# Kernel tuning notes

Hardware: AMD Instinct MI355X
Metric: run time of the kernel (lower is better)

The kernel has to match this reference:

```python
import jax, jax.numpy as jnp
import numpy as np

P_F, P_E = 64, 64
S_F, S_E = 64, 64
W_F, W_E = 32, 32
FH, FO = 256, 128
PR_F, PR_E = 32, 32
VI_F, VI_E = 32, 32
RE_F, RE_E = 32, 32
H1, H2 = 64, 32
GH, NHEADS = 32, 4
DH = PR_E + VI_E + RE_E + P_E + S_E  # 224, hypernetwork input dim
FUSE_IN = 2 * P_E + 2 * S_E + W_E    # 288
N_COLL = 200000
M_NODES = 2048


def setup_inputs() -> dict:
    key = jax.random.key(0)
    ks = jax.random.split(key, 40)
    rn = lambda k, s, sc=1.0: jax.random.normal(k, s, jnp.float32) * sc
    W = 0.05
    inp = {
        'x_u_profile': rn(ks[0], (1, P_F)),
        'x_u_shopping': rn(ks[1], (1, S_F)),
        'x_u_workplace': rn(ks[2], (1, W_F)),
        'x_u_colleague_p': rn(ks[3], (N_COLL, P_F)),
        'x_u_colleague_s': rn(ks[4], (N_COLL, S_F)),
        'x_h_property': rn(ks[5], (1, PR_F)),
        'x_h_vicinity': rn(ks[6], (1, VI_F)),
        'x_h_reachability': rn(ks[7], (1, RE_F)),
        'x_h_neighborhood_p': rn(ks[8], (M_NODES, P_F)),
        'x_h_neighborhood_s': rn(ks[9], (M_NODES, S_F)),
        'x_h_neighborhood_g': jax.random.randint(ks[10], (M_NODES, M_NODES), 0, 2, jnp.int32),
        'W_up': rn(ks[11], (P_F, P_E), W), 'b_up': jnp.zeros((P_E,), jnp.float32),
        'W_us': rn(ks[12], (S_F, S_E), W), 'b_us': jnp.zeros((S_E,), jnp.float32),
        'W_uw': rn(ks[13], (W_F, W_E), W), 'b_uw': jnp.zeros((W_E,), jnp.float32),
        'v_w': rn(ks[14], (2 * (P_E + S_E), 1), W),
        'W_f1': rn(ks[15], (FUSE_IN, FH), W), 'b_f1': jnp.zeros((FH,), jnp.float32),
        'W_f2': rn(ks[16], (FH, FO), W), 'b_f2': jnp.zeros((FO,), jnp.float32),
        'W_m1': rn(ks[17], (FO, DH * H1), W), 'b_m1': jnp.zeros((DH * H1,), jnp.float32),
        'W_m2': rn(ks[18], (FO, H1 * H2), W), 'b_m2': jnp.zeros((H1 * H2,), jnp.float32),
        'W_m3': rn(ks[19], (FO, H2), W), 'b_m3': jnp.zeros((H2,), jnp.float32),
        'W_hp': rn(ks[20], (PR_F, PR_E), W), 'b_hp': jnp.zeros((PR_E,), jnp.float32),
        'W_hv': rn(ks[21], (VI_F, VI_E), W), 'b_hv': jnp.zeros((VI_E,), jnp.float32),
        'W_hr': rn(ks[22], (RE_F, RE_E), W), 'b_hr': jnp.zeros((RE_E,), jnp.float32),
        'Wg': rn(ks[23], (NHEADS, P_E + S_E, GH), W),
        'ag': rn(ks[24], (NHEADS, 2 * GH, 1), W),
        'Wo': rn(ks[25], (NHEADS * GH, P_E + S_E), W),
        'ao': rn(ks[26], (2 * (P_E + S_E), 1), W),
    }
    return inp


def _forward(x_u_profile, x_u_shopping, x_u_workplace, x_u_colleague_p, x_u_colleague_s,
             x_h_property, x_h_vicinity, x_h_reachability,
             x_h_neighborhood_p, x_h_neighborhood_s,
             W_up, b_up, W_us, b_us, W_uw, b_uw, v_w,
             W_f1, b_f1, W_f2, b_f2,
             W_m1, b_m1, W_m2, b_m2, W_m3, b_m3,
             W_hp, b_hp, W_hv, b_hv, W_hr, b_hr,
             Wg, ag, Wo, ao, adj):
    celu, relu = jax.nn.celu, jax.nn.relu
    # user embeddings (batch = 1)
    u_p = celu(x_u_profile @ W_up + b_up)    # [1, P_E]
    u_s = celu(x_u_shopping @ W_us + b_us)   # [1, S_E]
    u_w = celu(x_u_workplace @ W_uw + b_uw)  # [1, W_E]
    # colleague embeddings (shared embedding weights)
    c_p = celu(x_u_colleague_p @ W_up + b_up)  # [N, P_E]
    c_s = celu(x_u_colleague_s @ W_us + b_us)  # [N, S_E]
    n = c_p.shape[0]
    # expand user (shopping, profile) to colleague set and attend
    exp = jnp.concatenate([jnp.broadcast_to(u_s, (n, S_E)),
                           jnp.broadcast_to(u_p, (n, P_E))], axis=1)
    concat = jnp.concatenate([exp, c_p, c_s], axis=1)        # [N, 2*(P_E+S_E)]
    atten = jax.nn.softmax(concat @ v_w, axis=0)             # [N, 1]
    coll = jnp.concatenate([c_p, c_s], axis=1)               # [N, P_E+S_E]
    x_coll = (atten.T @ coll) / n                            # [1, P_E+S_E]
    # user fusion
    fu = jnp.concatenate([u_p, u_s, u_w, x_coll], axis=1)    # [1, FUSE_IN]
    x_u = celu(celu(fu @ W_f1 + b_f1) @ W_f2 + b_f2)         # [1, FO]
    # hypernetwork-generated weights
    w1 = celu(x_u @ W_m1 + b_m1).reshape(DH, H1)
    w2 = celu(x_u @ W_m2 + b_m2).reshape(H1, H2)
    w3 = celu(x_u @ W_m3 + b_m3).reshape(H2, 1)
    # house embeddings
    h_p = celu(x_h_property @ W_hp + b_hp)
    h_v = celu(x_h_vicinity @ W_hv + b_hv)
    h_r = celu(x_h_reachability @ W_hr + b_hr)
    # neighborhood GAT over dense adjacency
    n_p = celu(x_h_neighborhood_p @ W_up + b_up)
    n_s = celu(x_h_neighborhood_s @ W_us + b_us)
    gx = jnp.concatenate([n_p, n_s], axis=1)                 # [M, P_E+S_E]
    mask = adj > 0

    def gat_layer(x, Wl, al):
        h = x @ Wl                                            # [M, F]
        f = h.shape[1]
        f1 = h @ al[:f]                                       # [M, 1]
        f2 = h @ al[f:]                                       # [M, 1]
        e = jax.nn.leaky_relu(f1 + f2.T, 0.2)                 # [M, M]
        e = jnp.where(mask, e, -1e9)
        att = jax.nn.softmax(e, axis=1)
        return att @ h

    heads = jax.vmap(lambda Wl, al: jax.nn.elu(gat_layer(gx, Wl, al)))(Wg, ag)  # [H, M, GH]
    hcat = jnp.transpose(heads, (1, 0, 2)).reshape(gx.shape[0], NHEADS * GH)
    gat_out = jax.nn.elu(gat_layer(hcat, Wo, ao))             # [M, P_E+S_E]
    neigh = gat_out.mean(axis=0, keepdims=True)               # [1, P_E+S_E]
    x_h = jnp.concatenate([h_p, h_v, h_r, neigh], axis=1)     # [1, DH]
    # meta_fcn: per-user generated MLP applied to house features
    return jax.nn.sigmoid(relu(relu(x_h @ w1) @ w2) @ w3)     # [1, 1]


def reference(x_u_profile, x_u_shopping, x_u_workplace, x_u_colleague_p, x_u_colleague_s,
              x_h_property, x_h_vicinity, x_h_reachability,
              x_h_neighborhood_p, x_h_neighborhood_s, x_h_neighborhood_g,
              W_up, b_up, W_us, b_us, W_uw, b_uw, v_w,
              W_f1, b_f1, W_f2, b_f2,
              W_m1, b_m1, W_m2, b_m2, W_m3, b_m3,
              W_hp, b_hp, W_hv, b_hv, W_hr, b_hr,
              Wg, ag, Wo, ao):
    return _forward(x_u_profile, x_u_shopping, x_u_workplace, x_u_colleague_p, x_u_colleague_s,
                    x_h_property, x_h_vicinity, x_h_reachability,
                    x_h_neighborhood_p, x_h_neighborhood_s,
                    W_up, b_up, W_us, b_us, W_uw, b_uw, v_w,
                    W_f1, b_f1, W_f2, b_f2,
                    W_m1, b_m1, W_m2, b_m2, W_m3, b_m3,
                    W_hp, b_hp, W_hv, b_hv, W_hr, b_hr,
                    Wg, ag, Wo, ao, x_h_neighborhood_g)
```

## Files before the change

kernel.cpp:

```cpp
#include <hip/hip_runtime.h>
#include <math.h>

#define N_COLL 200000

typedef const float* fp;
typedef __attribute__((ext_vector_type(8))) short bf16x8;
typedef __attribute__((ext_vector_type(4))) float f32x4;
typedef __attribute__((ext_vector_type(4))) short s16x4;

#define WS_UP    0
#define WS_US    64
#define WS_UW    128
#define WS_HP    160
#define WS_HV    192
#define WS_HR    224
#define WS_XU    384
#define WS_W1    512
#define WS_W2    14848
#define WS_W3    16896
#define WS_NEIGH 16928
#define WS_CSUM  18976
#define WS_GX    23552
#define WS_HT1   285696
#define WS_F1G   416768
#define WS_F2G   424960
#define WS_HCAT  433152
#define WS_HT2   695296
#define WS_F1O   826368
#define WS_F2O   828416
#define WS_MASK  830464

__device__ __forceinline__ float celu1(float x){
    return fmaxf(x, 0.f) + __expf(fminf(x, 0.f)) - 1.f;
}
__device__ __forceinline__ float rl(float x, int k){
    return __int_as_float(__builtin_amdgcn_readlane(__float_as_int(x), k));
}
__device__ __forceinline__ short f2bf(float f){
    return (short)(__float_as_uint(f) >> 16);
}
__device__ __forceinline__ bf16x8 pack8(f32x4 a, f32x4 b){
    bf16x8 r;
    r[0]=f2bf(a[0]); r[1]=f2bf(a[1]); r[2]=f2bf(a[2]); r[3]=f2bf(a[3]);
    r[4]=f2bf(b[0]); r[5]=f2bf(b[1]); r[6]=f2bf(b[2]); r[7]=f2bf(b[3]);
    return r;
}

__global__ __launch_bounds__(256) void kA(
    fp Xcp, fp Xcs, fp vw,
    fp xup, fp xus, fp xuw, fp xhp, fp xhv, fp xhr,
    fp Wup, fp bup, fp Wus, fp bus, fp Wuw, fp buw,
    fp Whp, fp bhp, fp Whv, fp bhv, fp Whr, fp bhr,
    fp Xnp, fp Xns, const int* __restrict__ adj, float* ws)
{
    __shared__ float sRed[528];
    const int t = threadIdx.x;
    const int b = blockIdx.x;
    const int lane = t & 63, wv = t >> 6;
    const int q = lane >> 4, c16 = lane & 15;
    if (b < 1024){
        bf16x8 B[2][2][4];
        float bias[8], vv[8];
        #pragma unroll
        for (int mat = 0; mat < 2; ++mat){
            fp W = mat ? Wus : Wup;
            #pragma unroll
            for (int ks = 0; ks < 2; ++ks)
                #pragma unroll
                for (int ct = 0; ct < 4; ++ct){
                    bf16x8 f;
                    #pragma unroll
                    for (int j = 0; j < 8; ++j)
                        f[j] = f2bf(W[(ks*32 + q*8 + j)*64 + ct*16 + c16]);
                    B[mat][ks][ct] = f;
                }
        }
        #pragma unroll
        for (int tt = 0; tt < 8; ++tt){
            int gcol = tt*16 + c16;
            bias[tt] = (tt < 4) ? bup[gcol] : bus[gcol-64];
            vv[tt]   = vw[128 + gcol];
        }
        const int wave = b*4 + wv;
        float accw[8] = {0,0,0,0,0,0,0,0};
        float accl = 0.f;
        int rt = wave;
        f32x4 L[8];
        {
            int row = rt*16 + c16;
            const float* xp = Xcp + row*64 + q*8;
            const float* xs = Xcs + row*64 + q*8;
            L[0]=*(const f32x4*)(xp);    L[1]=*(const f32x4*)(xp+4);
            L[2]=*(const f32x4*)(xp+32); L[3]=*(const f32x4*)(xp+36);
            L[4]=*(const f32x4*)(xs);    L[5]=*(const f32x4*)(xs+4);
            L[6]=*(const f32x4*)(xs+32); L[7]=*(const f32x4*)(xs+36);
        }
        while (rt < 12500){
            int nrt = rt + 4096;
            f32x4 N[8];
            if (nrt < 12500){
                int row = nrt*16 + c16;
                const float* xp = Xcp + row*64 + q*8;
                const float* xs = Xcs + row*64 + q*8;
                N[0]=*(const f32x4*)(xp);    N[1]=*(const f32x4*)(xp+4);
                N[2]=*(const f32x4*)(xp+32); N[3]=*(const f32x4*)(xp+36);
                N[4]=*(const f32x4*)(xs);    N[5]=*(const f32x4*)(xs+4);
                N[6]=*(const f32x4*)(xs+32); N[7]=*(const f32x4*)(xs+36);
            }
            bf16x8 Ap0 = pack8(L[0],L[1]);
            bf16x8 Ap1 = pack8(L[2],L[3]);
            bf16x8 As0 = pack8(L[4],L[5]);
            bf16x8 As1 = pack8(L[6],L[7]);
            float cel[8][4];
            float logit[4] = {0,0,0,0};
            #pragma unroll
            for (int tt = 0; tt < 8; ++tt){
                int ct = tt & 3;
                f32x4 c = {0.f,0.f,0.f,0.f};
                if (tt < 4){
                    c = __builtin_amdgcn_mfma_f32_16x16x32_bf16(Ap0, B[0][0][ct], c, 0,0,0);
                    c = __builtin_amdgcn_mfma_f32_16x16x32_bf16(Ap1, B[0][1][ct], c, 0,0,0);
                } else {
                    c = __builtin_amdgcn_mfma_f32_16x16x32_bf16(As0, B[1][0][ct], c, 0,0,0);
                    c = __builtin_amdgcn_mfma_f32_16x16x32_bf16(As1, B[1][1][ct], c, 0,0,0);
                }
                #pragma unroll
                for (int r = 0; r < 4; ++r){
                    float v = celu1(c[r] + bias[tt]);
                    cel[tt][r] = v;
                    logit[r] = fmaf(v, vv[tt], logit[r]);
                }
            }
            #pragma unroll
            for (int d = 1; d < 16; d <<= 1){
                #pragma unroll
                for (int r = 0; r < 4; ++r) logit[r] += __shfl_xor(logit[r], d);
            }
            float p[4];
            #pragma unroll
            for (int r = 0; r < 4; ++r){ p[r] = __expf(logit[r]); accl += p[r]; }
            #pragma unroll
            for (int tt = 0; tt < 8; ++tt)
                #pragma unroll
                for (int r = 0; r < 4; ++r) accw[tt] = fmaf(p[r], cel[tt][r], accw[tt]);
            #pragma unroll
            for (int i = 0; i < 8; ++i) L[i] = N[i];
            rt = nrt;
        }
        #pragma unroll
        for (int tt = 0; tt < 8; ++tt){
            accw[tt] += __shfl_xor(accw[tt], 16);
            accw[tt] += __shfl_xor(accw[tt], 32);
        }
        accl += __shfl_xor(accl, 16);
        accl += __shfl_xor(accl, 32);
        if (q == 0){
            #pragma unroll
            for (int tt = 0; tt < 8; ++tt) sRed[wv*132 + tt*16 + c16] = accw[tt];
        }
        if (lane == 0) sRed[wv*132 + 128] = accl;
        __syncthreads();
        if (t < 129){
            float s = sRed[t] + sRed[132+t] + sRed[264+t] + sRed[396+t];
            atomicAdd(ws + WS_CSUM + (b & 31)*132 + t, s);
        }
    } else if (b < 1280){
        unsigned* mb = (unsigned*)(ws + WS_MASK);
        #pragma unroll
        for (int s = 0; s < 2; ++s){
            int idx = (b-1024)*512 + s*256 + t;
            const int* a = adj + (idx>>6)*2048 + (idx&63)*32;
            unsigned bits = 0u;
            #pragma unroll 8
            for (int j = 0; j < 32; ++j) bits |= (a[j] > 0 ? 1u : 0u) << j;
            mb[idx] = bits;
        }
    } else if (b < 1408){
        int wave = ((b-1280)<<2) | wv;
        for (int r = wave; r < 2048; r += 512){
            float xp = Xnp[(r<<6)+lane], xs = Xns[(r<<6)+lane];
            float cp = bup[lane], cs = bus[lane];
            #pragma unroll 8
            for (int k = 0; k < 64; ++k){
                cp = fmaf(rl(xp,k), Wup[(k<<6)+lane], cp);
                cs = fmaf(rl(xs,k), Wus[(k<<6)+lane], cs);
            }
            ws[WS_GX + (r<<7) + lane]      = celu1(cp);
            ws[WS_GX + (r<<7) + 64 + lane] = celu1(cs);
        }
    } else {
        if (t < 64){
            float acc = bup[t];
            for (int k = 0; k < 64; ++k) acc = fmaf(xup[k], Wup[k*64+t], acc);
            ws[WS_UP+t] = celu1(acc);
        } else if (t < 128){
            int j = t-64; float acc = bus[j];
            for (int k = 0; k < 64; ++k) acc = fmaf(xus[k], Wus[k*64+j], acc);
            ws[WS_US+j] = celu1(acc);
        } else if (t < 160){
            int j = t-128; float acc = buw[j];
            for (int k = 0; k < 32; ++k) acc = fmaf(xuw[k], Wuw[k*32+j], acc);
            ws[WS_UW+j] = celu1(acc);
        } else if (t < 192){
            int j = t-160; float acc = bhp[j];
            for (int k = 0; k < 32; ++k) acc = fmaf(xhp[k], Whp[k*32+j], acc);
            ws[WS_HP+j] = celu1(acc);
        } else if (t < 224){
            int j = t-192; float acc = bhv[j];
            for (int k = 0; k < 32; ++k) acc = fmaf(xhv[k], Whv[k*32+j], acc);
            ws[WS_HV+j] = celu1(acc);
        } else {
            int j = t-224; float acc = bhr[j];
            for (int k = 0; k < 32; ++k) acc = fmaf(xhr[k], Whr[k*32+j], acc);
            ws[WS_HR+j] = celu1(acc);
        }
    }
}

__global__ __launch_bounds__(256) void kB(fp Wg, fp ag, fp Wf1, fp bf1, fp Wf2, fp bf2, float* ws){
    __shared__ float smem[673];
    const int t = threadIdx.x;
    const int b = blockIdx.x;
    const int lane = t & 63, wv = t >> 6;
    const int q = lane >> 4, c16 = lane & 15;
    if (b < 128){
        int rt = b, w = wv;
        bf16x8 A[4];
        const float* gxr = ws + WS_GX + (rt*16 + c16)*128;
        #pragma unroll
        for (int kt = 0; kt < 4; ++kt)
            A[kt] = pack8(*(const f32x4*)(gxr + kt*32 + q*8),
                          *(const f32x4*)(gxr + kt*32 + q*8 + 4));
        unsigned short* ht = (unsigned short*)(ws + WS_HT1);
        float f1p[4] = {0,0,0,0}, f2p[4] = {0,0,0,0};
        #pragma unroll
        for (int ct = 0; ct < 2; ++ct){
            int g = ct*16 + c16;
            f32x4 c = {0,0,0,0};
            #pragma unroll
            for (int kt = 0; kt < 4; ++kt){
                bf16x8 Bf;
                #pragma unroll
                for (int j = 0; j < 8; ++j)
                    Bf[j] = f2bf(Wg[w*4096 + (kt*32 + q*8 + j)*32 + g]);
                c = __builtin_amdgcn_mfma_f32_16x16x32_bf16(A[kt], Bf, c, 0,0,0);
            }
            int col = w*32 + g;
            s16x4 pk;
            pk[0]=f2bf(c[0]); pk[1]=f2bf(c[1]); pk[2]=f2bf(c[2]); pk[3]=f2bf(c[3]);
            *(s16x4*)(ht + col*2048 + rt*16 + q*4) = pk;
            float aga = ag[w*64 + g], agb = ag[w*64 + 32 + g];
            #pragma unroll
            for (int r = 0; r < 4; ++r){
                f1p[r] = fmaf(c[r], aga, f1p[r]);
                f2p[r] = fmaf(c[r], agb, f2p[r]);
            }
        }
        #pragma unroll
        for (int d = 1; d < 16; d <<= 1){
            #pragma unroll
            for (int r = 0; r < 4; ++r){
                f1p[r] += __shfl_xor(f1p[r], d);
                f2p[r] += __shfl_xor(f2p[r], d);
            }
        }
        if (c16 == 0){
            #pragma unroll
            for (int r = 0; r < 4; ++r){
                ws[WS_F1G + (w<<11) + rt*16 + q*4 + r] = f1p[r];
                ws[WS_F2G + (w<<11) + rt*16 + q*4 + r] = f2p[r];
            }
        }
    } else {
        float* fu  = smem;
        float* hid = smem + 288;
        float* cs  = smem + 544;
        if (t < 129){
            float s = 0.f;
            #pragma unroll
            for (int k = 0; k < 32; ++k) s += ws[WS_CSUM + k*132 + t];
            cs[t] = s;
        }
        if (t < 64)       fu[t] = ws[WS_UP + t];
        else if (t < 128) fu[t] = ws[WS_US + t-64];
        else if (t < 160) fu[t] = ws[WS_UW + t-128];
        __syncthreads();
        if (t < 128) fu[160 + t] = cs[t] / (cs[128] * (float)N_COLL);
        __syncthreads();
        float acc = bf1[t];
        for (int k = 0; k < 288; ++k) acc = fmaf(fu[k], Wf1[k*256+t], acc);
        hid[t] = celu1(acc);
        __syncthreads();
        if (t < 128){
            float a2 = bf2[t];
            for (int k = 0; k < 256; ++k) a2 = fmaf(hid[k], Wf2[k*128+t], a2);
            ws[WS_XU + t] = celu1(a2);
        }
    }
}

__global__ __launch_bounds__(256) void kC(fp Wm1, fp bm1, fp Wm2, fp bm2, fp Wm3, fp bm3, float* ws){
    __shared__ float smem[2112];
    const int t = threadIdx.x;
    const int b = blockIdx.x;
    const int lane = t & 63, wv = t >> 6;
    const int q = lane >> 4, c16 = lane & 15;
    if (b < 512){
        float* Cs = smem;
        float* Sp = smem + 2048;
        int w = wv;
        int rt = b >> 2, h = b & 3;
        int row = rt*16 + c16;
        const unsigned* mb = (const unsigned*)(ws + WS_MASK) + row*64;
        const unsigned short* HT = (const unsigned short*)(ws + WS_HT1) + h*32*2048;
        float f1 = ws[WS_F1G + (h<<11) + row];
        const float* f2 = ws + WS_F2G + (h<<11);
        f32x4 c0 = {0,0,0,0}, c1 = {0,0,0,0};
        float S = 0.f;
        for (int kt = w*16; kt < w*16 + 16; ++kt){
            unsigned m32 = mb[kt];
            const float* f2p = f2 + kt*32 + q*8;
            f32x4 fa = *(const f32x4*)(f2p);
            f32x4 fb = *(const f32x4*)(f2p+4);
            bf16x8 A;
            #pragma unroll
            for (int j = 0; j < 8; ++j){
                float e = f1 + ((j<4) ? fa[j] : fb[j-4]);
                e = fmaxf(e, 0.2f*e);
                float p = ((m32 >> (q*8+j)) & 1u) ? __expf(e) : 0.f;
                unsigned short pb = (unsigned short)(__float_as_uint(p) >> 16);
                A[j] = (short)pb;
                S += __uint_as_float(((unsigned)pb) << 16);
            }
            bf16x8 B0 = *(const bf16x8*)(HT + (c16)*2048    + kt*32 + q*8);
            bf16x8 B1 = *(const bf16x8*)(HT + (16+c16)*2048 + kt*32 + q*8);
            c0 = __builtin_amdgcn_mfma_f32_16x16x32_bf16(A, B0, c0, 0,0,0);
            c1 = __builtin_amdgcn_mfma_f32_16x16x32_bf16(A, B1, c1, 0,0,0);
        }
        S += __shfl_xor(S, 16);
        S += __shfl_xor(S, 32);
        if (q == 0) Sp[w*16 + c16] = S;
        #pragma unroll
        for (int r = 0; r < 4; ++r){
            Cs[w*512 + (q*4+r)*32 + c16]      = c0[r];
            Cs[w*512 + (q*4+r)*32 + 16 + c16] = c1[r];
        }
        __syncthreads();
        for (int ee = t; ee < 512; ee += 256){
            int r = ee >> 5, cc = ee & 31;
            float v = Cs[r*32+cc] + Cs[512 + r*32+cc] + Cs[1024 + r*32+cc] + Cs[1536 + r*32+cc];
            float Ss = Sp[r] + Sp[16+r] + Sp[32+r] + Sp[48+r];
            ws[WS_HCAT + (rt*16 + r)*128 + h*32 + cc] = celu1(v / Ss);
        }
    } else {
        float* xu = smem;
        if (t < 128) xu[t] = ws[WS_XU + t];
        __syncthreads();
        int j = (b - 512)*256 + t;
        if (j < 14336){
            float acc = bm1[j];
            for (int k = 0; k < 128; ++k) acc = fmaf(xu[k], Wm1[k*14336 + j], acc);
            ws[WS_W1 + j] = celu1(acc);
        } else if (j < 16384){
            int j2 = j - 14336;
            float acc = bm2[j2];
            for (int k = 0; k < 128; ++k) acc = fmaf(xu[k], Wm2[k*2048 + j2], acc);
            ws[WS_W2 + j2] = celu1(acc);
        } else if (j < 16416){
            int j3 = j - 16384;
            float acc = bm3[j3];
            for (int k = 0; k < 128; ++k) acc = fmaf(xu[k], Wm3[k*32 + j3], acc);
            ws[WS_W3 + j3] = celu1(acc);
        }
    }
}

__global__ __launch_bounds__(256) void kD(fp Wo, fp ao, float* ws){
    __shared__ float smem[128];
    const int t = threadIdx.x;
    const int lane = t & 63, wv = t >> 6;
    const int q = lane >> 4, c16 = lane & 15;
    int rt = blockIdx.x, w = wv;
    bf16x8 A[4];
    const float* hcr = ws + WS_HCAT + (rt*16 + c16)*128;
    #pragma unroll
    for (int kt = 0; kt < 4; ++kt)
        A[kt] = pack8(*(const f32x4*)(hcr + kt*32 + q*8),
                      *(const f32x4*)(hcr + kt*32 + q*8 + 4));
    unsigned short* ht = (unsigned short*)(ws + WS_HT2);
    float f1p[4] = {0,0,0,0}, f2p[4] = {0,0,0,0};
    #pragma unroll
    for (int ct = 0; ct < 2; ++ct){
        int col = w*32 + ct*16 + c16;
        f32x4 c = {0,0,0,0};
        #pragma unroll
        for (int kt = 0; kt < 4; ++kt){
            bf16x8 Bf;
            #pragma unroll
            for (int j = 0; j < 8; ++j)
                Bf[j] = f2bf(Wo[(kt*32 + q*8 + j)*128 + col]);
            c = __builtin_amdgcn_mfma_f32_16x16x32_bf16(A[kt], Bf, c, 0,0,0);
        }
        s16x4 pk;
        pk[0]=f2bf(c[0]); pk[1]=f2bf(c[1]); pk[2]=f2bf(c[2]); pk[3]=f2bf(c[3]);
        *(s16x4*)(ht + col*2048 + rt*16 + q*4) = pk;
        float aoa = ao[col], aob = ao[128 + col];
        #pragma unroll
        for (int r = 0; r < 4; ++r){
            f1p[r] = fmaf(c[r], aoa, f1p[r]);
            f2p[r] = fmaf(c[r], aob, f2p[r]);
        }
    }
    #pragma unroll
    for (int d = 1; d < 16; d <<= 1){
        #pragma unroll
        for (int r = 0; r < 4; ++r){
            f1p[r] += __shfl_xor(f1p[r], d);
            f2p[r] += __shfl_xor(f2p[r], d);
        }
    }
    if (c16 == 0){
        #pragma unroll
        for (int r = 0; r < 4; ++r){
            smem[w*16 + q*4 + r]      = f1p[r];
            smem[64 + w*16 + q*4 + r] = f2p[r];
        }
    }
    __syncthreads();
    if (t < 16){
        float s = smem[t] + smem[16+t] + smem[32+t] + smem[48+t];
        float u = smem[64+t] + smem[80+t] + smem[96+t] + smem[112+t];
        ws[WS_F1O + rt*16 + t] = s;
        ws[WS_F2O + rt*16 + t] = u;
    }
}

__global__ __launch_bounds__(256) void kE(float* ws){
    __shared__ float Cs[4][16][64];
    __shared__ float Sp[4][16];
    __shared__ float colp[4][64];
    const int t = threadIdx.x;
    const int lane = t & 63, wv = t >> 6;
    const int q = lane >> 4, c16 = lane & 15;
    int rt = blockIdx.x >> 1, half = blockIdx.x & 1;
    int w = wv;
    int row = rt*16 + c16;
    const unsigned* mb = (const unsigned*)(ws + WS_MASK) + row*64;
    const unsigned short* HT = (const unsigned short*)(ws + WS_HT2);
    float f1 = ws[WS_F1O + row];
    const float* f2 = ws + WS_F2O;
    f32x4 c[4];
    #pragma unroll
    for (int nt = 0; nt < 4; ++nt) c[nt] = (f32x4){0,0,0,0};
    float S = 0.f;
    for (int kt = w*16; kt < w*16 + 16; ++kt){
        unsigned m32 = mb[kt];
        const float* f2p = f2 + kt*32 + q*8;
        f32x4 fa = *(const f32x4*)(f2p);
        f32x4 fb = *(const f32x4*)(f2p+4);
        bf16x8 A;
        #pragma unroll
        for (int j = 0; j < 8; ++j){
            float e = f1 + ((j<4) ? fa[j] : fb[j-4]);
            e = fmaxf(e, 0.2f*e);
            float p = ((m32 >> (q*8+j)) & 1u) ? __expf(e) : 0.f;
            unsigned short pb = (unsigned short)(__float_as_uint(p) >> 16);
            A[j] = (short)pb;
            S += __uint_as_float(((unsigned)pb) << 16);
        }
        #pragma unroll
        for (int nt = 0; nt < 4; ++nt){
            int col16 = half*4 + nt;
            bf16x8 B = *(const bf16x8*)(HT + (col16*16 + c16)*2048 + kt*32 + q*8);
            c[nt] = __builtin_amdgcn_mfma_f32_16x16x32_bf16(A, B, c[nt], 0,0,0);
        }
    }
    S += __shfl_xor(S, 16);
    S += __shfl_xor(S, 32);
    if (q == 0) Sp[w][c16] = S;
    #pragma unroll
    for (int nt = 0; nt < 4; ++nt)
        #pragma unroll
        for (int r = 0; r < 4; ++r)
            Cs[w][q*4+r][nt*16+c16] = c[nt][r];
    __syncthreads();
    int col = t & 63, grp = t >> 6;
    float part = 0.f;
    for (int r = grp*4; r < grp*4 + 4; ++r){
        float v = Cs[0][r][col] + Cs[1][r][col] + Cs[2][r][col] + Cs[3][r][col];
        float Ss = Sp[0][r] + Sp[1][r] + Sp[2][r] + Sp[3][r];
        part += celu1(v / Ss);
    }
    colp[grp][col] = part;
    __syncthreads();
    if (t < 64){
        float s = colp[0][t] + colp[1][t] + colp[2][t] + colp[3][t];
        atomicAdd(ws + WS_NEIGH + (blockIdx.x & 15)*128 + half*64 + t, s);
    }
}

__global__ __launch_bounds__(256) void kF(float* ws, float* out){
    __shared__ float xh[224], r1[64], r2[32];
    int t = threadIdx.x;
    if (t < 32)       xh[t]      = ws[WS_HP + t];
    else if (t < 64)  xh[t]      = ws[WS_HV + t-32];
    else if (t < 96)  xh[t]      = ws[WS_HR + t-64];
    if (t < 128){
        float s = 0.f;
        #pragma unroll
        for (int k = 0; k < 16; ++k) s += ws[WS_NEIGH + k*128 + t];
        xh[96 + t] = s * (1.f/2048.f);
    }
    __syncthreads();
    if (t < 64){
        float acc = 0.f;
        for (int k = 0; k < 224; ++k) acc = fmaf(xh[k], ws[WS_W1 + k*64 + t], acc);
        r1[t] = fmaxf(acc, 0.f);
    }
    __syncthreads();
    if (t < 32){
        float acc = 0.f;
        for (int k = 0; k < 64; ++k) acc = fmaf(r1[k], ws[WS_W2 + k*32 + t], acc);
        r2[t] = fmaxf(acc, 0.f);
    }
    __syncthreads();
    if (t == 0){
        float acc = 0.f;
        for (int k = 0; k < 32; ++k) acc = fmaf(r2[k], ws[WS_W3 + k], acc);
        out[0] = 1.f / (1.f + __expf(-acc));
    }
}

extern "C" void kernel_launch(void* const* d_in, const int* in_sizes, int n_in,
                              void* d_out, int out_size, void* d_ws, size_t ws_size,
                              hipStream_t stream)
{
    fp xup = (fp)d_in[0],  xus = (fp)d_in[1],  xuw = (fp)d_in[2];
    fp Xcp = (fp)d_in[3],  Xcs = (fp)d_in[4];
    fp xhp = (fp)d_in[5],  xhv = (fp)d_in[6],  xhr = (fp)d_in[7];
    fp Xnp = (fp)d_in[8],  Xns = (fp)d_in[9];
    const int* adj = (const int*)d_in[10];
    fp Wup = (fp)d_in[11], bup = (fp)d_in[12];
    fp Wus = (fp)d_in[13], bus = (fp)d_in[14];
    fp Wuw = (fp)d_in[15], buw = (fp)d_in[16];
    fp vw  = (fp)d_in[17];
    fp Wf1 = (fp)d_in[18], bf1 = (fp)d_in[19];
    fp Wf2 = (fp)d_in[20], bf2 = (fp)d_in[21];
    fp Wm1 = (fp)d_in[22], bm1 = (fp)d_in[23];
    fp Wm2 = (fp)d_in[24], bm2 = (fp)d_in[25];
    fp Wm3 = (fp)d_in[26], bm3 = (fp)d_in[27];
    fp Whp = (fp)d_in[28], bhp = (fp)d_in[29];
    fp Whv = (fp)d_in[30], bhv = (fp)d_in[31];
    fp Whr = (fp)d_in[32], bhr = (fp)d_in[33];
    fp Wg  = (fp)d_in[34], ag  = (fp)d_in[35];
    fp Wo  = (fp)d_in[36], ao  = (fp)d_in[37];
    float* ws = (float*)d_ws;
    float* out = (float*)d_out;

    hipMemsetAsync((char*)d_ws + WS_NEIGH*sizeof(float), 0, 6272*sizeof(float), stream);

    kA<<<1409, 256, 0, stream>>>(Xcp,Xcs,vw, xup,xus,xuw,xhp,xhv,xhr,
                                 Wup,bup,Wus,bus,Wuw,buw,Whp,bhp,Whv,bhv,Whr,bhr,
                                 Xnp,Xns, adj, ws);
    kB<<<129, 256, 0, stream>>>(Wg, ag, Wf1,bf1,Wf2,bf2, ws);
    kC<<<577, 256, 0, stream>>>(Wm1,bm1,Wm2,bm2,Wm3,bm3, ws);
    kD<<<128, 256, 0, stream>>>(Wo, ao, ws);
    kE<<<256, 256, 0, stream>>>(ws);
    kF<<<1, 256, 0, stream>>>(ws, out);
}
```

Baseline: 288.6 us.

## Split colleague attention pass across kernels to overlap with graph stages

The 200k-row colleague attention-pooling pass is split into three tile ranges. They run alongside the GAT stages in kA, kB and kC instead of entirely in kA. The user-fusion MLP moves into kD and the hypernetwork into kE, after all colleague partial sums are complete. The aim is to fill idle CUs during the small graph kernels, at the cost of dropping the register double-buffered prefetch and adding larger grids.

Measured after the change: 302.7 us. 4.9% more time.

```diff
diff --git a/kernel.cpp b/kernel.cpp
--- a/kernel.cpp
+++ b/kernel.cpp
@@ -46,6 +46,96 @@
     return r;
 }
 
+__device__ __forceinline__ void coll_slice(
+    fp Xp, fp Xs, fp Wup, fp bup, fp Wus, fp bus, fp vw, float* ws,
+    float* sRed, int t, int wave, int nwaves, int t0, int t1, int bank)
+{
+    const int lane = t & 63, wv = t >> 6;
+    const int q = lane >> 4, c16 = lane & 15;
+    bf16x8 B[2][2][4];
+    float bias[8], vv[8];
+    #pragma unroll
+    for (int mat = 0; mat < 2; ++mat){
+        fp W = mat ? Wus : Wup;
+        #pragma unroll
+        for (int ks = 0; ks < 2; ++ks)
+            #pragma unroll
+            for (int ct = 0; ct < 4; ++ct){
+                bf16x8 f;
+                #pragma unroll
+                for (int j = 0; j < 8; ++j)
+                    f[j] = f2bf(W[(ks*32 + q*8 + j)*64 + ct*16 + c16]);
+                B[mat][ks][ct] = f;
+            }
+    }
+    #pragma unroll
+    for (int tt = 0; tt < 8; ++tt){
+        int gcol = tt*16 + c16;
+        bias[tt] = (tt < 4) ? bup[gcol] : bus[gcol-64];
+        vv[tt]   = vw[128 + gcol];
+    }
+    float accw[8] = {0,0,0,0,0,0,0,0};
+    float accl = 0.f;
+    for (int rt = t0 + wave; rt < t1; rt += nwaves){
+        int row = rt*16 + c16;
+        const float* xp = Xp + row*64 + q*8;
+        const float* xs = Xs + row*64 + q*8;
+        bf16x8 Ap0 = pack8(*(const f32x4*)(xp),    *(const f32x4*)(xp+4));
+        bf16x8 Ap1 = pack8(*(const f32x4*)(xp+32), *(const f32x4*)(xp+36));
+        bf16x8 As0 = pack8(*(const f32x4*)(xs),    *(const f32x4*)(xs+4));
+        bf16x8 As1 = pack8(*(const f32x4*)(xs+32), *(const f32x4*)(xs+36));
+        float cel[8][4];
+        float logit[4] = {0,0,0,0};
+        #pragma unroll
+        for (int tt = 0; tt < 8; ++tt){
+            int ct = tt & 3;
+            f32x4 c = {0.f,0.f,0.f,0.f};
+            if (tt < 4){
+                c = __builtin_amdgcn_mfma_f32_16x16x32_bf16(Ap0, B[0][0][ct], c, 0,0,0);
+                c = __builtin_amdgcn_mfma_f32_16x16x32_bf16(Ap1, B[0][1][ct], c, 0,0,0);
+            } else {
+                c = __builtin_amdgcn_mfma_f32_16x16x32_bf16(As0, B[1][0][ct], c, 0,0,0);
+                c = __builtin_amdgcn_mfma_f32_16x16x32_bf16(As1, B[1][1][ct], c, 0,0,0);
+            }
+            #pragma unroll
+            for (int r = 0; r < 4; ++r){
+                float v = celu1(c[r] + bias[tt]);
+                cel[tt][r] = v;
+                logit[r] = fmaf(v, vv[tt], logit[r]);
+            }
+        }
+        #pragma unroll
+        for (int d = 1; d < 16; d <<= 1){
+            #pragma unroll
+            for (int r = 0; r < 4; ++r) logit[r] += __shfl_xor(logit[r], d);
+        }
+        float p[4];
+        #pragma unroll
+        for (int r = 0; r < 4; ++r){ p[r] = __expf(logit[r]); accl += p[r]; }
+        #pragma unroll
+        for (int tt = 0; tt < 8; ++tt)
+            #pragma unroll
+            for (int r = 0; r < 4; ++r) accw[tt] = fmaf(p[r], cel[tt][r], accw[tt]);
+    }
+    #pragma unroll
+    for (int tt = 0; tt < 8; ++tt){
+        accw[tt] += __shfl_xor(accw[tt], 16);
+        accw[tt] += __shfl_xor(accw[tt], 32);
+    }
+    accl += __shfl_xor(accl, 16);
+    accl += __shfl_xor(accl, 32);
+    if (q == 0){
+        #pragma unroll
+        for (int tt = 0; tt < 8; ++tt) sRed[wv*132 + tt*16 + c16] = accw[tt];
+    }
+    if (lane == 0) sRed[wv*132 + 128] = accl;
+    __syncthreads();
+    if (t < 129){
+        float s = sRed[t] + sRed[132+t] + sRed[264+t] + sRed[396+t];
+        atomicAdd(ws + WS_CSUM + bank*132 + t, s);
+    }
+}
+
 __global__ __launch_bounds__(256) void kA(
     fp Xcp, fp Xcs, fp vw,
     fp xup, fp xus, fp xuw, fp xhp, fp xhv, fp xhr,
@@ -57,113 +147,8 @@
     const int t = threadIdx.x;
     const int b = blockIdx.x;
     const int lane = t & 63, wv = t >> 6;
-    const int q = lane >> 4, c16 = lane & 15;
     if (b < 1024){
-        bf16x8 B[2][2][4];
-        float bias[8], vv[8];
-        #pragma unroll
-        for (int mat = 0; mat < 2; ++mat){
-            fp W = mat ? Wus : Wup;
-            #pragma unroll
-            for (int ks = 0; ks < 2; ++ks)
-                #pragma unroll
-                for (int ct = 0; ct < 4; ++ct){
-                    bf16x8 f;
-                    #pragma unroll
-                    for (int j = 0; j < 8; ++j)
-                        f[j] = f2bf(W[(ks*32 + q*8 + j)*64 + ct*16 + c16]);
-                    B[mat][ks][ct] = f;
-                }
-        }
-        #pragma unroll
-        for (int tt = 0; tt < 8; ++tt){
-            int gcol = tt*16 + c16;
-            bias[tt] = (tt < 4) ? bup[gcol] : bus[gcol-64];
-            vv[tt]   = vw[128 + gcol];
-        }
-        const int wave = b*4 + wv;
-        float accw[8] = {0,0,0,0,0,0,0,0};
-        float accl = 0.f;
-        int rt = wave;
-        f32x4 L[8];
-        {
-            int row = rt*16 + c16;
-            const float* xp = Xcp + row*64 + q*8;
-            const float* xs = Xcs + row*64 + q*8;
-            L[0]=*(const f32x4*)(xp);    L[1]=*(const f32x4*)(xp+4);
-            L[2]=*(const f32x4*)(xp+32); L[3]=*(const f32x4*)(xp+36);
-            L[4]=*(const f32x4*)(xs);    L[5]=*(const f32x4*)(xs+4);
-            L[6]=*(const f32x4*)(xs+32); L[7]=*(const f32x4*)(xs+36);
-        }
-        while (rt < 12500){
-            int nrt = rt + 4096;
-            f32x4 N[8];
-            if (nrt < 12500){
-                int row = nrt*16 + c16;
-                const float* xp = Xcp + row*64 + q*8;
-                const float* xs = Xcs + row*64 + q*8;
-                N[0]=*(const f32x4*)(xp);    N[1]=*(const f32x4*)(xp+4);
-                N[2]=*(const f32x4*)(xp+32); N[3]=*(const f32x4*)(xp+36);
-                N[4]=*(const f32x4*)(xs);    N[5]=*(const f32x4*)(xs+4);
-                N[6]=*(const f32x4*)(xs+32); N[7]=*(const f32x4*)(xs+36);
-            }
-            bf16x8 Ap0 = pack8(L[0],L[1]);
-            bf16x8 Ap1 = pack8(L[2],L[3]);
-            bf16x8 As0 = pack8(L[4],L[5]);
-            bf16x8 As1 = pack8(L[6],L[7]);
-            float cel[8][4];
-            float logit[4] = {0,0,0,0};
-            #pragma unroll
-            for (int tt = 0; tt < 8; ++tt){
-                int ct = tt & 3;
-                f32x4 c = {0.f,0.f,0.f,0.f};
-                if (tt < 4){
-                    c = __builtin_amdgcn_mfma_f32_16x16x32_bf16(Ap0, B[0][0][ct], c, 0,0,0);
-                    c = __builtin_amdgcn_mfma_f32_16x16x32_bf16(Ap1, B[0][1][ct], c, 0,0,0);
-                } else {
-                    c = __builtin_amdgcn_mfma_f32_16x16x32_bf16(As0, B[1][0][ct], c, 0,0,0);
-                    c = __builtin_amdgcn_mfma_f32_16x16x32_bf16(As1, B[1][1][ct], c, 0,0,0);
-                }
-                #pragma unroll
-                for (int r = 0; r < 4; ++r){
-                    float v = celu1(c[r] + bias[tt]);
-                    cel[tt][r] = v;
-                    logit[r] = fmaf(v, vv[tt], logit[r]);
-                }
-            }
-            #pragma unroll
-            for (int d = 1; d < 16; d <<= 1){
-                #pragma unroll
-                for (int r = 0; r < 4; ++r) logit[r] += __shfl_xor(logit[r], d);
-            }
-            float p[4];
-            #pragma unroll
-            for (int r = 0; r < 4; ++r){ p[r] = __expf(logit[r]); accl += p[r]; }
-            #pragma unroll
-            for (int tt = 0; tt < 8; ++tt)
-                #pragma unroll
-                for (int r = 0; r < 4; ++r) accw[tt] = fmaf(p[r], cel[tt][r], accw[tt]);
-            #pragma unroll
-            for (int i = 0; i < 8; ++i) L[i] = N[i];
-            rt = nrt;
-        }
-        #pragma unroll
-        for (int tt = 0; tt < 8; ++tt){
-            accw[tt] += __shfl_xor(accw[tt], 16);
-            accw[tt] += __shfl_xor(accw[tt], 32);
-        }
-        accl += __shfl_xor(accl, 16);
-        accl += __shfl_xor(accl, 32);
-        if (q == 0){
-            #pragma unroll
-            for (int tt = 0; tt < 8; ++tt) sRed[wv*132 + tt*16 + c16] = accw[tt];
-        }
-        if (lane == 0) sRed[wv*132 + 128] = accl;
-        __syncthreads();
-        if (t < 129){
-            float s = sRed[t] + sRed[132+t] + sRed[264+t] + sRed[396+t];
-            atomicAdd(ws + WS_CSUM + (b & 31)*132 + t, s);
-        }
+        coll_slice(Xcp,Xcs,Wup,bup,Wus,bus,vw,ws,sRed,t, b*4+wv, 4096, 0, 4167, b&31);
     } else if (b < 1280){
         unsigned* mb = (unsigned*)(ws + WS_MASK);
         #pragma unroll
@@ -217,8 +202,11 @@
     }
 }
 
-__global__ __launch_bounds__(256) void kB(fp Wg, fp ag, fp Wf1, fp bf1, fp Wf2, fp bf2, float* ws){
-    __shared__ float smem[673];
+__global__ __launch_bounds__(256) void kB(
+    fp Xcp, fp Xcs, fp vw, fp Wup, fp bup, fp Wus, fp bus,
+    fp Wg, fp ag, float* ws)
+{
+    __shared__ float sRed[528];
     const int t = threadIdx.x;
     const int b = blockIdx.x;
     const int lane = t & 63, wv = t >> 6;
@@ -272,34 +260,13 @@
             }
         }
     } else {
-        float* fu  = smem;
-        float* hid = smem + 288;
-        float* cs  = smem + 544;
-        if (t < 129){
-            float s = 0.f;
-            #pragma unroll
-            for (int k = 0; k < 32; ++k) s += ws[WS_CSUM + k*132 + t];
-            cs[t] = s;
-        }
-        if (t < 64)       fu[t] = ws[WS_UP + t];
-        else if (t < 128) fu[t] = ws[WS_US + t-64];
-        else if (t < 160) fu[t] = ws[WS_UW + t-128];
-        __syncthreads();
-        if (t < 128) fu[160 + t] = cs[t] / (cs[128] * (float)N_COLL);
-        __syncthreads();
-        float acc = bf1[t];
-        for (int k = 0; k < 288; ++k) acc = fmaf(fu[k], Wf1[k*256+t], acc);
-        hid[t] = celu1(acc);
-        __syncthreads();
-        if (t < 128){
-            float a2 = bf2[t];
-            for (int k = 0; k < 256; ++k) a2 = fmaf(hid[k], Wf2[k*128+t], a2);
-            ws[WS_XU + t] = celu1(a2);
-        }
-    }
-}
-
-__global__ __launch_bounds__(256) void kC(fp Wm1, fp bm1, fp Wm2, fp bm2, fp Wm3, fp bm3, float* ws){
+        coll_slice(Xcp,Xcs,Wup,bup,Wus,bus,vw,ws,sRed,t, (b-128)*4+wv, 2048, 4167, 8334, b&31);
+    }
+}
+
+__global__ __launch_bounds__(256) void kC(
+    fp Xcp, fp Xcs, fp vw, fp Wup, fp bup, fp Wus, fp bus, float* ws)
+{
     __shared__ float smem[2112];
     const int t = threadIdx.x;
     const int b = blockIdx.x;
@@ -353,10 +320,168 @@
             ws[WS_HCAT + (rt*16 + r)*128 + h*32 + cc] = celu1(v / Ss);
         }
     } else {
+        coll_slice(Xcp,Xcs,Wup,bup,Wus,bus,vw,ws,smem,t, (b-512)*4+wv, 2048, 8334, 12500, b&31);
+    }
+}
+
+__global__ __launch_bounds__(256) void kD(fp Wo, fp ao, fp Wf1, fp bf1, fp Wf2, fp bf2, float* ws){
+    __shared__ float smem[673];
+    const int t = threadIdx.x;
+    const int b = blockIdx.x;
+    const int lane = t & 63, wv = t >> 6;
+    const int q = lane >> 4, c16 = lane & 15;
+    if (b < 128){
+        int rt = b, w = wv;
+        bf16x8 A[4];
+        const float* hcr = ws + WS_HCAT + (rt*16 + c16)*128;
+        #pragma unroll
+        for (int kt = 0; kt < 4; ++kt)
+            A[kt] = pack8(*(const f32x4*)(hcr + kt*32 + q*8),
+                          *(const f32x4*)(hcr + kt*32 + q*8 + 4));
+        unsigned short* ht = (unsigned short*)(ws + WS_HT2);
+        float f1p[4] = {0,0,0,0}, f2p[4] = {0,0,0,0};
+        #pragma unroll
+        for (int ct = 0; ct < 2; ++ct){
+            int col = w*32 + ct*16 + c16;
+            f32x4 c = {0,0,0,0};
+            #pragma unroll
+            for (int kt = 0; kt < 4; ++kt){
+                bf16x8 Bf;
+                #pragma unroll
+                for (int j = 0; j < 8; ++j)
+                    Bf[j] = f2bf(Wo[(kt*32 + q*8 + j)*128 + col]);
+                c = __builtin_amdgcn_mfma_f32_16x16x32_bf16(A[kt], Bf, c, 0,0,0);
+            }
+            s16x4 pk;
+            pk[0]=f2bf(c[0]); pk[1]=f2bf(c[1]); pk[2]=f2bf(c[2]); pk[3]=f2bf(c[3]);
+            *(s16x4*)(ht + col*2048 + rt*16 + q*4) = pk;
+            float aoa = ao[col], aob = ao[128 + col];
+            #pragma unroll
+            for (int r = 0; r < 4; ++r){
+                f1p[r] = fmaf(c[r], aoa, f1p[r]);
+                f2p[r] = fmaf(c[r], aob, f2p[r]);
+            }
+        }
+        #pragma unroll
+        for (int d = 1; d < 16; d <<= 1){
+            #pragma unroll
+            for (int r = 0; r < 4; ++r){
+                f1p[r] += __shfl_xor(f1p[r], d);
+                f2p[r] += __shfl_xor(f2p[r], d);
+            }
+        }
+        if (c16 == 0){
+            #pragma unroll
+            for (int r = 0; r < 4; ++r){
+                smem[w*16 + q*4 + r]      = f1p[r];
+                smem[64 + w*16 + q*4 + r] = f2p[r];
+            }
+        }
+        __syncthreads();
+        if (t < 16){
+            float s = smem[t] + smem[16+t] + smem[32+t] + smem[48+t];
+            float u = smem[64+t] + smem[80+t] + smem[96+t] + smem[112+t];
+            ws[WS_F1O + rt*16 + t] = s;
+            ws[WS_F2O + rt*16 + t] = u;
+        }
+    } else {
+        float* fu  = smem;
+        float* hid = smem + 288;
+        float* cs  = smem + 544;
+        if (t < 129){
+            float s = 0.f;
+            #pragma unroll
+            for (int k = 0; k < 32; ++k) s += ws[WS_CSUM + k*132 + t];
+            cs[t] = s;
+        }
+        if (t < 64)       fu[t] = ws[WS_UP + t];
+        else if (t < 128) fu[t] = ws[WS_US + t-64];
+        else if (t < 160) fu[t] = ws[WS_UW + t-128];
+        __syncthreads();
+        if (t < 128) fu[160 + t] = cs[t] / (cs[128] * (float)N_COLL);
+        __syncthreads();
+        float acc = bf1[t];
+        for (int k = 0; k < 288; ++k) acc = fmaf(fu[k], Wf1[k*256+t], acc);
+        hid[t] = celu1(acc);
+        __syncthreads();
+        if (t < 128){
+            float a2 = bf2[t];
+            for (int k = 0; k < 256; ++k) a2 = fmaf(hid[k], Wf2[k*128+t], a2);
+            ws[WS_XU + t] = celu1(a2);
+        }
+    }
+}
+
+__global__ __launch_bounds__(256) void kE(fp Wm1, fp bm1, fp Wm2, fp bm2, fp Wm3, fp bm3, float* ws){
+    __shared__ float smem[4416];
+    const int t = threadIdx.x;
+    const int b = blockIdx.x;
+    const int lane = t & 63, wv = t >> 6;
+    const int q = lane >> 4, c16 = lane & 15;
+    if (b < 256){
+        float* Cs   = smem;
+        float* Sp   = smem + 4096;
+        float* colp = smem + 4160;
+        int rt = b >> 1, half = b & 1;
+        int w = wv;
+        int row = rt*16 + c16;
+        const unsigned* mb = (const unsigned*)(ws + WS_MASK) + row*64;
+        const unsigned short* HT = (const unsigned short*)(ws + WS_HT2);
+        float f1 = ws[WS_F1O + row];
+        const float* f2 = ws + WS_F2O;
+        f32x4 c[4];
+        #pragma unroll
+        for (int nt = 0; nt < 4; ++nt) c[nt] = (f32x4){0,0,0,0};
+        float S = 0.f;
+        for (int kt = w*16; kt < w*16 + 16; ++kt){
+            unsigned m32 = mb[kt];
+            const float* f2p = f2 + kt*32 + q*8;
+            f32x4 fa = *(const f32x4*)(f2p);
+            f32x4 fb = *(const f32x4*)(f2p+4);
+            bf16x8 A;
+            #pragma unroll
+            for (int j = 0; j < 8; ++j){
+                float e = f1 + ((j<4) ? fa[j] : fb[j-4]);
+                e = fmaxf(e, 0.2f*e);
+                float p = ((m32 >> (q*8+j)) & 1u) ? __expf(e) : 0.f;
+                unsigned short pb = (unsigned short)(__float_as_uint(p) >> 16);
+                A[j] = (short)pb;
+                S += __uint_as_float(((unsigned)pb) << 16);
+            }
+            #pragma unroll
+            for (int nt = 0; nt < 4; ++nt){
+                int col16 = half*4 + nt;
+                bf16x8 B = *(const bf16x8*)(HT + (col16*16 + c16)*2048 + kt*32 + q*8);
+                c[nt] = __builtin_amdgcn_mfma_f32_16x16x32_bf16(A, B, c[nt], 0,0,0);
+            }
+        }
+        S += __shfl_xor(S, 16);
+        S += __shfl_xor(S, 32);
+        if (q == 0) Sp[w*16 + c16] = S;
+        #pragma unroll
+        for (int nt = 0; nt < 4; ++nt)
+            #pragma unroll
+            for (int r = 0; r < 4; ++r)
+                Cs[w*1024 + (q*4+r)*64 + nt*16 + c16] = c[nt][r];
+        __syncthreads();
+        int col = t & 63, grp = t >> 6;
+        float part = 0.f;
+        for (int r = grp*4; r < grp*4 + 4; ++r){
+            float v = Cs[r*64+col] + Cs[1024 + r*64+col] + Cs[2048 + r*64+col] + Cs[3072 + r*64+col];
+            float Ss = Sp[r] + Sp[16+r] + Sp[32+r] + Sp[48+r];
+            part += celu1(v / Ss);
+        }
+        colp[grp*64 + col] = part;
+        __syncthreads();
+        if (t < 64){
+            float s = colp[t] + colp[64+t] + colp[128+t] + colp[192+t];
+            atomicAdd(ws + WS_NEIGH + (b & 15)*128 + half*64 + t, s);
+        }
+    } else {
         float* xu = smem;
         if (t < 128) xu[t] = ws[WS_XU + t];
         __syncthreads();
-        int j = (b - 512)*256 + t;
+        int j = (b - 256)*256 + t;
         if (j < 14336){
             float acc = bm1[j];
             for (int k = 0; k < 128; ++k) acc = fmaf(xu[k], Wm1[k*14336 + j], acc);
@@ -372,130 +497,6 @@
             for (int k = 0; k < 128; ++k) acc = fmaf(xu[k], Wm3[k*32 + j3], acc);
             ws[WS_W3 + j3] = celu1(acc);
         }
-    }
-}
-
-__global__ __launch_bounds__(256) void kD(fp Wo, fp ao, float* ws){
-    __shared__ float smem[128];
-    const int t = threadIdx.x;
-    const int lane = t & 63, wv = t >> 6;
-    const int q = lane >> 4, c16 = lane & 15;
-    int rt = blockIdx.x, w = wv;
-    bf16x8 A[4];
-    const float* hcr = ws + WS_HCAT + (rt*16 + c16)*128;
-    #pragma unroll
-    for (int kt = 0; kt < 4; ++kt)
-        A[kt] = pack8(*(const f32x4*)(hcr + kt*32 + q*8),
-                      *(const f32x4*)(hcr + kt*32 + q*8 + 4));
-    unsigned short* ht = (unsigned short*)(ws + WS_HT2);
-    float f1p[4] = {0,0,0,0}, f2p[4] = {0,0,0,0};
-    #pragma unroll
-    for (int ct = 0; ct < 2; ++ct){
-        int col = w*32 + ct*16 + c16;
-        f32x4 c = {0,0,0,0};
-        #pragma unroll
-        for (int kt = 0; kt < 4; ++kt){
-            bf16x8 Bf;
-            #pragma unroll
-            for (int j = 0; j < 8; ++j)
-                Bf[j] = f2bf(Wo[(kt*32 + q*8 + j)*128 + col]);
-            c = __builtin_amdgcn_mfma_f32_16x16x32_bf16(A[kt], Bf, c, 0,0,0);
-        }
-        s16x4 pk;
-        pk[0]=f2bf(c[0]); pk[1]=f2bf(c[1]); pk[2]=f2bf(c[2]); pk[3]=f2bf(c[3]);
-        *(s16x4*)(ht + col*2048 + rt*16 + q*4) = pk;
-        float aoa = ao[col], aob = ao[128 + col];
-        #pragma unroll
-        for (int r = 0; r < 4; ++r){
-            f1p[r] = fmaf(c[r], aoa, f1p[r]);
-            f2p[r] = fmaf(c[r], aob, f2p[r]);
-        }
-    }
-    #pragma unroll
-    for (int d = 1; d < 16; d <<= 1){
-        #pragma unroll
-        for (int r = 0; r < 4; ++r){
-            f1p[r] += __shfl_xor(f1p[r], d);
-            f2p[r] += __shfl_xor(f2p[r], d);
-        }
-    }
-    if (c16 == 0){
-        #pragma unroll
-        for (int r = 0; r < 4; ++r){
-            smem[w*16 + q*4 + r]      = f1p[r];
-            smem[64 + w*16 + q*4 + r] = f2p[r];
-        }
-    }
-    __syncthreads();
-    if (t < 16){
-        float s = smem[t] + smem[16+t] + smem[32+t] + smem[48+t];
-        float u = smem[64+t] + smem[80+t] + smem[96+t] + smem[112+t];
-        ws[WS_F1O + rt*16 + t] = s;
-        ws[WS_F2O + rt*16 + t] = u;
-    }
-}
-
-__global__ __launch_bounds__(256) void kE(float* ws){
-    __shared__ float Cs[4][16][64];
-    __shared__ float Sp[4][16];
-    __shared__ float colp[4][64];
-    const int t = threadIdx.x;
-    const int lane = t & 63, wv = t >> 6;
-    const int q = lane >> 4, c16 = lane & 15;
-    int rt = blockIdx.x >> 1, half = blockIdx.x & 1;
-    int w = wv;
-    int row = rt*16 + c16;
-    const unsigned* mb = (const unsigned*)(ws + WS_MASK) + row*64;
-    const unsigned short* HT = (const unsigned short*)(ws + WS_HT2);
-    float f1 = ws[WS_F1O + row];
-    const float* f2 = ws + WS_F2O;
-    f32x4 c[4];
-    #pragma unroll
-    for (int nt = 0; nt < 4; ++nt) c[nt] = (f32x4){0,0,0,0};
-    float S = 0.f;
-    for (int kt = w*16; kt < w*16 + 16; ++kt){
-        unsigned m32 = mb[kt];
-        const float* f2p = f2 + kt*32 + q*8;
-        f32x4 fa = *(const f32x4*)(f2p);
-        f32x4 fb = *(const f32x4*)(f2p+4);
-        bf16x8 A;
-        #pragma unroll
-        for (int j = 0; j < 8; ++j){
-            float e = f1 + ((j<4) ? fa[j] : fb[j-4]);
-            e = fmaxf(e, 0.2f*e);
-            float p = ((m32 >> (q*8+j)) & 1u) ? __expf(e) : 0.f;
-            unsigned short pb = (unsigned short)(__float_as_uint(p) >> 16);
-            A[j] = (short)pb;
-            S += __uint_as_float(((unsigned)pb) << 16);
-        }
-        #pragma unroll
-        for (int nt = 0; nt < 4; ++nt){
-            int col16 = half*4 + nt;
-            bf16x8 B = *(const bf16x8*)(HT + (col16*16 + c16)*2048 + kt*32 + q*8);
-            c[nt] = __builtin_amdgcn_mfma_f32_16x16x32_bf16(A, B, c[nt], 0,0,0);
-        }
-    }
-    S += __shfl_xor(S, 16);
-    S += __shfl_xor(S, 32);
-    if (q == 0) Sp[w][c16] = S;
-    #pragma unroll
-    for (int nt = 0; nt < 4; ++nt)
-        #pragma unroll
-        for (int r = 0; r < 4; ++r)
-            Cs[w][q*4+r][nt*16+c16] = c[nt][r];
-    __syncthreads();
-    int col = t & 63, grp = t >> 6;
-    float part = 0.f;
-    for (int r = grp*4; r < grp*4 + 4; ++r){
-        float v = Cs[0][r][col] + Cs[1][r][col] + Cs[2][r][col] + Cs[3][r][col];
-        float Ss = Sp[0][r] + Sp[1][r] + Sp[2][r] + Sp[3][r];
-        part += celu1(v / Ss);
-    }
-    colp[grp][col] = part;
-    __syncthreads();
-    if (t < 64){
-        float s = colp[0][t] + colp[1][t] + colp[2][t] + colp[3][t];
-        atomicAdd(ws + WS_NEIGH + (blockIdx.x & 15)*128 + half*64 + t, s);
     }
 }
 
@@ -562,9 +563,9 @@
     kA<<<1409, 256, 0, stream>>>(Xcp,Xcs,vw, xup,xus,xuw,xhp,xhv,xhr,
                                  Wup,bup,Wus,bus,Wuw,buw,Whp,bhp,Whv,bhv,Whr,bhr,
                                  Xnp,Xns, adj, ws);
-    kB<<<129, 256, 0, stream>>>(Wg, ag, Wf1,bf1,Wf2,bf2, ws);
-    kC<<<577, 256, 0, stream>>>(Wm1,bm1,Wm2,bm2,Wm3,bm3, ws);
-    kD<<<128, 256, 0, stream>>>(Wo, ao, ws);
-    kE<<<256, 256, 0, stream>>>(ws);
+    kB<<<640, 256, 0, stream>>>(Xcp,Xcs,vw,Wup,bup,Wus,bus, Wg,ag, ws);
+    kC<<<1024, 256, 0, stream>>>(Xcp,Xcs,vw,Wup,bup,Wus,bus, ws);
+    kD<<<129, 256, 0, stream>>>(Wo,ao, Wf1,bf1,Wf2,bf2, ws);
+    kE<<<321, 256, 0, stream>>>(Wm1,bm1,Wm2,bm2,Wm3,bm3, ws);
     kF<<<1, 256, 0, stream>>>(ws, out);
 }
```
